# Kernel optimization log

Measured on AMD Instinct MI355X. Metric: run time of the kernel, lower is better.

Reference implementation:

```python
import jax, jax.numpy as jnp
import numpy as np

H, W = 720, 1280
NVIEWS, FEAT, HIDDEN = 30, 8, 64
GRIDS = ((16, 16, 8), (12, 12, 8), (8, 8, 4))  # (grid_X, grid_Y, grid_W) per scale
RGB2GRAY = np.array([0.299, 0.587, 0.114], dtype=np.float32)


def setup_inputs() -> dict:
    key = jax.random.key(0)
    ks = jax.random.split(key, 8)
    inp = {"rgb": jax.random.uniform(ks[0], (H, W, 3), jnp.float32)}
    for i, (gx, gy, gl) in enumerate(GRIDS):
        # grids: (N, C, L, Hg, Wg) per the docstring '(N, 12, L, H, W)'
        inp[f"grids{i}"] = jax.random.normal(ks[1 + i], (NVIEWS, FEAT, gl, gy, gx), jnp.float32) * 0.1
    din = len(GRIDS) * FEAT
    inp["w1"] = jax.random.normal(ks[4], (din, HIDDEN), jnp.float32) / np.sqrt(din)
    inp["w2"] = jax.random.normal(ks[5], (HIDDEN, HIDDEN), jnp.float32) / np.sqrt(HIDDEN)
    inp["w3"] = jax.random.normal(ks[6], (HIDDEN, 12), jnp.float32) / np.sqrt(HIDDEN)
    inp["cam_idx"] = 5
    return inp


def _slice_grid(g, rgb):
    """Trilinear bilateral-grid slicing (grid_sample 3D, align_corners=True).

    g: (C, L, Hg, Wg) grid for one view; rgb: (h, w, 3) in [0,1].
    Guidance z = gray luma; x/y are the normalized [0,1] image meshgrid.
    Returns (h, w, C).
    """
    C, L, Hg, Wg = g.shape
    h, w, _ = rgb.shape
    gray = jnp.clip(rgb @ jnp.asarray(RGB2GRAY, rgb.dtype), 0.0, 1.0)  # (h, w)
    # align_corners=True: normalized coord u in [0,1] -> u * (size - 1)
    x = jnp.broadcast_to(jnp.linspace(0.0, Wg - 1.0, w, dtype=rgb.dtype)[None, :], (h, w))
    y = jnp.broadcast_to(jnp.linspace(0.0, Hg - 1.0, h, dtype=rgb.dtype)[:, None], (h, w))
    z = gray * (L - 1.0)

    x0 = jnp.floor(x).astype(jnp.int32); x1 = jnp.minimum(x0 + 1, Wg - 1)
    y0 = jnp.floor(y).astype(jnp.int32); y1 = jnp.minimum(y0 + 1, Hg - 1)
    z0 = jnp.floor(z).astype(jnp.int32); z1 = jnp.minimum(z0 + 1, L - 1)
    wx, wy, wz = x - x0, y - y0, z - z0  # (h, w)

    def gat(zi, yi, xi):
        return g[:, zi, yi, xi]  # (C, h, w)

    c00 = gat(z0, y0, x0) * (1 - wx) + gat(z0, y0, x1) * wx
    c01 = gat(z0, y1, x0) * (1 - wx) + gat(z0, y1, x1) * wx
    c10 = gat(z1, y0, x0) * (1 - wx) + gat(z1, y0, x1) * wx
    c11 = gat(z1, y1, x0) * (1 - wx) + gat(z1, y1, x1) * wx
    c0 = c00 * (1 - wy) + c01 * wy
    c1 = c10 * (1 - wy) + c11 * wy
    out = c0 * (1 - wz) + c1 * wz  # (C, h, w)
    return jnp.transpose(out, (1, 2, 0))


def reference(rgb, grids0, grids1, grids2, w1, w2, w3, cam_idx):
    h, w, _ = rgb.shape
    feats = jnp.concatenate(
        [_slice_grid(g[cam_idx], rgb) for g in (grids0, grids1, grids2)], axis=-1
    )  # (h, w, 3*FEAT)
    hid = jnp.tanh(feats @ w1)
    hid = jnp.tanh(hid @ w2)
    out = hid @ w3  # (h, w, 12)
    return out.reshape(1, h, w, 3, 4)
```

## Files before the change

kernel.cpp:

```cpp
#include <hip/hip_runtime.h>
#include <hip/hip_bf16.h>

#define H_IMG 720
#define W_IMG 1280
#define NPIX (H_IMG * W_IMG)

typedef __attribute__((ext_vector_type(4))) float f32x4;
typedef __attribute__((ext_vector_type(8))) short short8;
typedef __attribute__((ext_vector_type(4))) short short4v;
typedef __attribute__((ext_vector_type(4))) uint u32x4;
typedef _Float16 h8 __attribute__((ext_vector_type(8)));

#define WPACK_BYTES (14 * 64 * 16)
#define GP0_OFF WPACK_BYTES
#define GP0_N (16 * 16 * 8 * 8)
#define GP1_OFF (GP0_OFF + GP0_N * 2)
#define GP1_N (12 * 12 * 8 * 8)
#define GP2_OFF (GP1_OFF + GP1_N * 2)
#define GP2_N (8 * 8 * 4 * 8)

#define XSTR 36

__device__ __forceinline__ uint pkh(float a, float b) {
  auto t = __builtin_amdgcn_cvt_pkrtz(a, b);
  return __builtin_bit_cast(uint, t);
}

__device__ __forceinline__ float tanh5(float x) {
  float e2 = __builtin_amdgcn_exp2f(x * 2.885390081777927f);
  return fmaf(-2.f, __builtin_amdgcn_rcpf(e2 + 1.f), 1.f);
}

__global__ __launch_bounds__(256) void prep_kernel(
    const float* __restrict__ g0, const float* __restrict__ g1, const float* __restrict__ g2,
    const float* __restrict__ w1, const float* __restrict__ w2, const float* __restrict__ w3,
    const int* __restrict__ cam, void* __restrict__ ws) {
  ushort* wpack = (ushort*)ws;
  ushort* gp0 = (ushort*)((char*)ws + GP0_OFF);
  ushort* gp1 = (ushort*)((char*)ws + GP1_OFF);
  ushort* gp2 = (ushort*)((char*)ws + GP2_OFF);
  const int ci = cam[0];
  const int tid = blockIdx.x * 256 + threadIdx.x;
  const int nth = gridDim.x * 256;

  for (int e = tid; e < GP0_N; e += nth) {
    int c = e & 7; int t = e >> 3; int z = t & 7; t >>= 3; int x = t & 15; int y = t >> 4;
    _Float16 hv = (_Float16)g0[ci * GP0_N + ((c * 8 + z) * 16 + y) * 16 + x];
    gp0[e] = __builtin_bit_cast(ushort, hv);
  }
  for (int e = tid; e < GP1_N; e += nth) {
    int c = e & 7; int t = e >> 3; int z = t & 7; t >>= 3; int x = t % 12; int y = t / 12;
    _Float16 hv = (_Float16)g1[ci * GP1_N + ((c * 8 + z) * 12 + y) * 12 + x];
    gp1[e] = __builtin_bit_cast(ushort, hv);
  }
  for (int e = tid; e < GP2_N; e += nth) {
    int c = e & 7; int t = e >> 3; int z = t & 3; t >>= 2; int x = t & 7; int y = t >> 3;
    _Float16 hv = (_Float16)g2[ci * GP2_N + ((c * 4 + z) * 8 + y) * 8 + x];
    gp2[e] = __builtin_bit_cast(ushort, hv);
  }

  for (int fl = tid; fl < 14 * 64; fl += nth) {
    int f = fl >> 6, lane = fl & 63;
    int g = lane >> 4, r = lane & 15;
    ushort* dh = wpack + fl * 8;
#pragma unroll
    for (int j = 0; j < 8; ++j) {
      float v = 0.f;
      if (f < 4) {
        int k = 8 * g + j, n = r + 16 * f;
        if (k < 24) v = w1[k * 64 + n];
      } else if (f < 12) {
        int q = f - 4, ks = q >> 2, mt = q & 3;
        v = w2[(8 * g + j + 32 * ks) * 64 + (r + 16 * mt)];
      } else {
        int ks = f - 12;
        if (r < 12) v = w3[(8 * g + j + 32 * ks) * 12 + r];
      }
      _Float16 hv = (_Float16)v;
      dh[j] = __builtin_bit_cast(ushort, hv);
    }
  }
}

template <int WG, int HG, int LG>
__device__ __forceinline__ h8 slice_h8(const h8* __restrict__ gp,
                                       int row, int col, float gray) {
  float x = (float)col * ((float)(WG - 1) / (float)(W_IMG - 1));
  float y = (float)row * ((float)(HG - 1) / (float)(H_IMG - 1));
  float z = gray * (float)(LG - 1);
  int x0 = (int)x, y0 = (int)y, z0 = (int)z;
  int x1 = min(x0 + 1, WG - 1), y1 = min(y0 + 1, HG - 1), z1 = min(z0 + 1, LG - 1);
  _Float16 wx = (_Float16)(x - (float)x0);
  _Float16 wy = (_Float16)(y - (float)y0);
  _Float16 wz = (_Float16)(z - (float)z0);
  h8 wx8 = {wx, wx, wx, wx, wx, wx, wx, wx};
  h8 wy8 = {wy, wy, wy, wy, wy, wy, wy, wy};
  h8 wz8 = {wz, wz, wz, wz, wz, wz, wz, wz};

  const h8* p00 = gp + (y0 * WG + x0) * LG;
  const h8* p01 = gp + (y0 * WG + x1) * LG;
  const h8* p10 = gp + (y1 * WG + x0) * LG;
  const h8* p11 = gp + (y1 * WG + x1) * LG;

  h8 a00 = p00[z0], a01 = p01[z0], a10 = p10[z0], a11 = p11[z0];
  h8 b00 = p00[z1], b01 = p01[z1], b10 = p10[z1], b11 = p11[z1];

  h8 xa = a00 + wx8 * (a01 - a00);
  h8 xb = a10 + wx8 * (a11 - a10);
  h8 ya = xa + wy8 * (xb - xa);
  h8 xc = b00 + wx8 * (b01 - b00);
  h8 xd = b10 + wx8 * (b11 - b10);
  h8 yb = xc + wy8 * (xd - xc);
  return ya + wz8 * (yb - ya);
}

__global__ __launch_bounds__(64, 4) void msnbat_kernel(
    const float* __restrict__ rgb, const void* __restrict__ ws, float* __restrict__ out) {
  __shared__ ushort W[64 * XSTR];
  uint* Wu = (uint*)W;

  const h8* wp = (const h8*)ws;
  const h8* gp0 = (const h8*)((const char*)ws + GP0_OFF);
  const h8* gp1 = (const h8*)((const char*)ws + GP1_OFF);
  const h8* gp2 = (const h8*)((const char*)ws + GP2_OFF);

  const int lane = threadIdx.x;
  const int g = lane >> 4, r = lane & 15;
  const int pixbase = blockIdx.x * 64;
  const int p = pixbase + lane;
  const int row = p / W_IMG;
  const int col = p - row * W_IMG;

  const float rr = rgb[p * 3 + 0], gg = rgb[p * 3 + 1], bb = rgb[p * 3 + 2];
  const float gray = fminf(fmaxf(rr * 0.299f + gg * 0.587f + bb * 0.114f, 0.f), 1.f);

  h8 f0 = slice_h8<16, 16, 8>(gp0, row, col, gray);
  h8 f1 = slice_h8<12, 12, 8>(gp1, row, col, gray);
  h8 f2 = slice_h8<8, 8, 4>(gp2, row, col, gray);

  {
    const int ub = lane * 18;
    u32x4 u0 = __builtin_bit_cast(u32x4, f0);
    u32x4 u1 = __builtin_bit_cast(u32x4, f1);
    u32x4 u2 = __builtin_bit_cast(u32x4, f2);
    *(uint2*)&Wu[ub + 0] = make_uint2(u0[0], u0[1]);
    *(uint2*)&Wu[ub + 2] = make_uint2(u0[2], u0[3]);
    *(uint2*)&Wu[ub + 4] = make_uint2(u1[0], u1[1]);
    *(uint2*)&Wu[ub + 6] = make_uint2(u1[2], u1[3]);
    *(uint2*)&Wu[ub + 8] = make_uint2(u2[0], u2[1]);
    *(uint2*)&Wu[ub + 10] = make_uint2(u2[2], u2[3]);
  }

  const h8 zero8 = (h8){0, 0, 0, 0, 0, 0, 0, 0};

  h8 B1[4];
#pragma unroll
  for (int nt = 0; nt < 4; ++nt) {
    short4v lo = *(short4v*)&W[(r + 16 * nt) * XSTR + 8 * g];
    short4v hi = *(short4v*)&W[(r + 16 * nt) * XSTR + 8 * g + 4];
    short8 s = __builtin_shufflevector(lo, hi, 0, 1, 2, 3, 4, 5, 6, 7);
    B1[nt] = (g < 3) ? __builtin_bit_cast(h8, s) : zero8;
  }

  h8 B2[2][4];
#pragma unroll
  for (int half = 0; half < 2; ++half) {
#pragma unroll
    for (int mtl = 0; mtl < 2; ++mtl) {
      const int mt = 2 * half + mtl;
      h8 A = wp[mt * 64 + lane];
      f32x4 a[4];
#pragma unroll
      for (int nt = 0; nt < 4; ++nt) a[nt] = (f32x4){0.f, 0.f, 0.f, 0.f};
#pragma unroll
      for (int nt = 0; nt < 4; ++nt)
        a[nt] = __builtin_amdgcn_mfma_f32_16x16x32_f16(A, B1[nt], a[nt], 0, 0, 0);
#pragma unroll
      for (int nt = 0; nt < 4; ++nt) {
        uint2 v = make_uint2(pkh(tanh5(a[nt][0]), tanh5(a[nt][1])),
                             pkh(tanh5(a[nt][2]), tanh5(a[nt][3])));
        *(uint2*)&Wu[(16 * nt + r) * 18 + 8 * mtl + 2 * g] = v;
      }
    }
#pragma unroll
    for (int nt = 0; nt < 4; ++nt) {
      short4v lo = *(short4v*)&W[(16 * nt + r) * XSTR + 8 * g];
      short4v hi = *(short4v*)&W[(16 * nt + r) * XSTR + 8 * g + 4];
      short8 s = __builtin_shufflevector(lo, hi, 0, 1, 2, 3, 4, 5, 6, 7);
      B2[half][nt] = __builtin_bit_cast(h8, s);
    }
  }

  h8 B3[2][4];
#pragma unroll
  for (int half = 0; half < 2; ++half) {
#pragma unroll
    for (int mtl = 0; mtl < 2; ++mtl) {
      const int mt = 2 * half + mtl;
      h8 A0 = wp[(4 + mt) * 64 + lane];
      h8 A1 = wp[(8 + mt) * 64 + lane];
      f32x4 a[4];
#pragma unroll
      for (int nt = 0; nt < 4; ++nt) a[nt] = (f32x4){0.f, 0.f, 0.f, 0.f};
#pragma unroll
      for (int nt = 0; nt < 4; ++nt)
        a[nt] = __builtin_amdgcn_mfma_f32_16x16x32_f16(A0, B2[0][nt], a[nt], 0, 0, 0);
#pragma unroll
      for (int nt = 0; nt < 4; ++nt)
        a[nt] = __builtin_amdgcn_mfma_f32_16x16x32_f16(A1, B2[1][nt], a[nt], 0, 0, 0);
#pragma unroll
      for (int nt = 0; nt < 4; ++nt) {
        uint2 v = make_uint2(pkh(tanh5(a[nt][0]), tanh5(a[nt][1])),
                             pkh(tanh5(a[nt][2]), tanh5(a[nt][3])));
        *(uint2*)&Wu[(16 * nt + r) * 18 + 8 * mtl + 2 * g] = v;
      }
    }
#pragma unroll
    for (int nt = 0; nt < 4; ++nt) {
      short4v lo = *(short4v*)&W[(16 * nt + r) * XSTR + 8 * g];
      short4v hi = *(short4v*)&W[(16 * nt + r) * XSTR + 8 * g + 4];
      short8 s = __builtin_shufflevector(lo, hi, 0, 1, 2, 3, 4, 5, 6, 7);
      B3[half][nt] = __builtin_bit_cast(h8, s);
    }
  }

  f32x4 acc3[4];
#pragma unroll
  for (int nt = 0; nt < 4; ++nt) acc3[nt] = (f32x4){0.f, 0.f, 0.f, 0.f};
  {
    h8 A0 = wp[12 * 64 + lane];
    h8 A1 = wp[13 * 64 + lane];
#pragma unroll
    for (int nt = 0; nt < 4; ++nt)
      acc3[nt] = __builtin_amdgcn_mfma_f32_16x16x32_f16(A0, B3[0][nt], acc3[nt], 0, 0, 0);
#pragma unroll
    for (int nt = 0; nt < 4; ++nt)
      acc3[nt] = __builtin_amdgcn_mfma_f32_16x16x32_f16(A1, B3[1][nt], acc3[nt], 0, 0, 0);
  }

  if (g < 3) {
#pragma unroll
    for (int nt = 0; nt < 4; ++nt) {
      int pix = pixbase + 16 * nt + r;
      *(f32x4*)(out + pix * 12 + 4 * g) = acc3[nt];
    }
  }
}

extern "C" void kernel_launch(void* const* d_in, const int* in_sizes, int n_in,
                              void* d_out, int out_size, void* d_ws, size_t ws_size,
                              hipStream_t stream) {
  const float* rgb = (const float*)d_in[0];
  const float* g0 = (const float*)d_in[1];
  const float* g1 = (const float*)d_in[2];
  const float* g2 = (const float*)d_in[3];
  const float* w1 = (const float*)d_in[4];
  const float* w2 = (const float*)d_in[5];
  const float* w3 = (const float*)d_in[6];
  const int* cam = (const int*)d_in[7];
  float* out = (float*)d_out;

  hipLaunchKernelGGL(prep_kernel, dim3(64), dim3(256), 0, stream,
                     g0, g1, g2, w1, w2, w3, cam, d_ws);
  hipLaunchKernelGGL(msnbat_kernel, dim3(NPIX / 64), dim3(64), 0, stream,
                     rgb, d_ws, out);
}
```

Measured before the change: 53.78 us.

## Widen LDS hidden buffer to full 64 rows and fold tanh scale into weights

Folds the 2/ln2 tanh pre-scale into the packed w1/w2 weights during prep, which removes one multiply per activation. The hidden-layer staging buffer is widened so each layer computes all four M-tiles before writing tanh results, replacing the earlier two-halves interleave. This lengthens MFMA chains and drops intermediate LDS round trips. In exchange, accumulator register pressure rises (16 f32x4 live per layer) and the LDS footprint roughly doubles, which may lower occupancy.

```diff
diff --git a/kernel.cpp b/kernel.cpp
--- a/kernel.cpp
+++ b/kernel.cpp
@@ -19,16 +19,23 @@
 #define GP2_OFF (GP1_OFF + GP1_N * 2)
 #define GP2_N (8 * 8 * 4 * 8)
 
-#define XSTR 36
+#define HSTR 68
+
+#define KSCALE 2.885390081777927f
 
 __device__ __forceinline__ uint pkh(float a, float b) {
   auto t = __builtin_amdgcn_cvt_pkrtz(a, b);
   return __builtin_bit_cast(uint, t);
 }
 
-__device__ __forceinline__ float tanh5(float x) {
-  float e2 = __builtin_amdgcn_exp2f(x * 2.885390081777927f);
-  return fmaf(-2.f, __builtin_amdgcn_rcpf(e2 + 1.f), 1.f);
+__device__ __forceinline__ float tanhu(float u) {
+  float e2 = __builtin_amdgcn_exp2f(u);
+  float r = __builtin_amdgcn_rcpf(e2 + 1.f);
+  return fmaf(-2.f, r, 1.f);
+}
+
+__device__ __forceinline__ uint2 tanh4(f32x4 u) {
+  return make_uint2(pkh(tanhu(u[0]), tanhu(u[1])), pkh(tanhu(u[2]), tanhu(u[3])));
 }
 
 __global__ __launch_bounds__(256) void prep_kernel(
@@ -68,10 +75,10 @@
       float v = 0.f;
       if (f < 4) {
         int k = 8 * g + j, n = r + 16 * f;
-        if (k < 24) v = w1[k * 64 + n];
+        if (k < 24) v = w1[k * 64 + n] * KSCALE;
       } else if (f < 12) {
         int q = f - 4, ks = q >> 2, mt = q & 3;
-        v = w2[(8 * g + j + 32 * ks) * 64 + (r + 16 * mt)];
+        v = w2[(8 * g + j + 32 * ks) * 64 + (r + 16 * mt)] * KSCALE;
       } else {
         int ks = f - 12;
         if (r < 12) v = w3[(8 * g + j + 32 * ks) * 12 + r];
@@ -116,7 +123,7 @@
 
 __global__ __launch_bounds__(64, 4) void msnbat_kernel(
     const float* __restrict__ rgb, const void* __restrict__ ws, float* __restrict__ out) {
-  __shared__ ushort W[64 * XSTR];
+  __shared__ ushort W[64 * HSTR];
   uint* Wu = (uint*)W;
 
   const h8* wp = (const h8*)ws;
@@ -139,7 +146,7 @@
   h8 f2 = slice_h8<8, 8, 4>(gp2, row, col, gray);
 
   {
-    const int ub = lane * 18;
+    const int ub = lane * (HSTR / 2);
     u32x4 u0 = __builtin_bit_cast(u32x4, f0);
     u32x4 u1 = __builtin_bit_cast(u32x4, f1);
     u32x4 u2 = __builtin_bit_cast(u32x4, f2);
@@ -156,86 +163,79 @@
   h8 B1[4];
 #pragma unroll
   for (int nt = 0; nt < 4; ++nt) {
-    short4v lo = *(short4v*)&W[(r + 16 * nt) * XSTR + 8 * g];
-    short4v hi = *(short4v*)&W[(r + 16 * nt) * XSTR + 8 * g + 4];
+    short4v lo = *(short4v*)&W[(r + 16 * nt) * HSTR + 8 * g];
+    short4v hi = *(short4v*)&W[(r + 16 * nt) * HSTR + 8 * g + 4];
     short8 s = __builtin_shufflevector(lo, hi, 0, 1, 2, 3, 4, 5, 6, 7);
     B1[nt] = (g < 3) ? __builtin_bit_cast(h8, s) : zero8;
   }
 
+  {
+    f32x4 a1[4][4];
+#pragma unroll
+    for (int mt = 0; mt < 4; ++mt)
+#pragma unroll
+      for (int nt = 0; nt < 4; ++nt) a1[mt][nt] = (f32x4){0.f, 0.f, 0.f, 0.f};
+#pragma unroll
+    for (int mt = 0; mt < 4; ++mt) {
+      h8 A = wp[mt * 64 + lane];
+#pragma unroll
+      for (int nt = 0; nt < 4; ++nt)
+        a1[mt][nt] = __builtin_amdgcn_mfma_f32_16x16x32_f16(A, B1[nt], a1[mt][nt], 0, 0, 0);
+    }
+#pragma unroll
+    for (int mt = 0; mt < 4; ++mt)
+#pragma unroll
+      for (int nt = 0; nt < 4; ++nt)
+        *(uint2*)&Wu[(16 * nt + r) * (HSTR / 2) + 8 * mt + 2 * g] = tanh4(a1[mt][nt]);
+  }
+
   h8 B2[2][4];
 #pragma unroll
-  for (int half = 0; half < 2; ++half) {
-#pragma unroll
-    for (int mtl = 0; mtl < 2; ++mtl) {
-      const int mt = 2 * half + mtl;
-      h8 A = wp[mt * 64 + lane];
-      f32x4 a[4];
-#pragma unroll
-      for (int nt = 0; nt < 4; ++nt) a[nt] = (f32x4){0.f, 0.f, 0.f, 0.f};
+  for (int ks = 0; ks < 2; ++ks)
+#pragma unroll
+    for (int nt = 0; nt < 4; ++nt) {
+      short4v lo = *(short4v*)&W[(16 * nt + r) * HSTR + 32 * ks + 8 * g];
+      short4v hi = *(short4v*)&W[(16 * nt + r) * HSTR + 32 * ks + 8 * g + 4];
+      short8 s = __builtin_shufflevector(lo, hi, 0, 1, 2, 3, 4, 5, 6, 7);
+      B2[ks][nt] = __builtin_bit_cast(h8, s);
+    }
+
+  {
+    f32x4 a2[4][4];
+#pragma unroll
+    for (int mt = 0; mt < 4; ++mt)
+#pragma unroll
+      for (int nt = 0; nt < 4; ++nt) a2[mt][nt] = (f32x4){0.f, 0.f, 0.f, 0.f};
+#pragma unroll
+    for (int ks = 0; ks < 2; ++ks)
+#pragma unroll
+      for (int mt = 0; mt < 4; ++mt) {
+        h8 A = wp[(4 + ks * 4 + mt) * 64 + lane];
+#pragma unroll
+        for (int nt = 0; nt < 4; ++nt)
+          a2[mt][nt] = __builtin_amdgcn_mfma_f32_16x16x32_f16(A, B2[ks][nt], a2[mt][nt], 0, 0, 0);
+      }
+#pragma unroll
+    for (int mt = 0; mt < 4; ++mt)
 #pragma unroll
       for (int nt = 0; nt < 4; ++nt)
-        a[nt] = __builtin_amdgcn_mfma_f32_16x16x32_f16(A, B1[nt], a[nt], 0, 0, 0);
-#pragma unroll
-      for (int nt = 0; nt < 4; ++nt) {
-        uint2 v = make_uint2(pkh(tanh5(a[nt][0]), tanh5(a[nt][1])),
-                             pkh(tanh5(a[nt][2]), tanh5(a[nt][3])));
-        *(uint2*)&Wu[(16 * nt + r) * 18 + 8 * mtl + 2 * g] = v;
-      }
-    }
+        *(uint2*)&Wu[(16 * nt + r) * (HSTR / 2) + 8 * mt + 2 * g] = tanh4(a2[mt][nt]);
+  }
+
+  f32x4 acc3[4];
+#pragma unroll
+  for (int nt = 0; nt < 4; ++nt) acc3[nt] = (f32x4){0.f, 0.f, 0.f, 0.f};
+#pragma unroll
+  for (int ks = 0; ks < 2; ++ks) {
+    h8 A = wp[(12 + ks) * 64 + lane];
 #pragma unroll
     for (int nt = 0; nt < 4; ++nt) {
-      short4v lo = *(short4v*)&W[(16 * nt + r) * XSTR + 8 * g];
-      short4v hi = *(short4v*)&W[(16 * nt + r) * XSTR + 8 * g + 4];
+      short4v lo = *(short4v*)&W[(16 * nt + r) * HSTR + 32 * ks + 8 * g];
+      short4v hi = *(short4v*)&W[(16 * nt + r) * HSTR + 32 * ks + 8 * g + 4];
       short8 s = __builtin_shufflevector(lo, hi, 0, 1, 2, 3, 4, 5, 6, 7);
-      B2[half][nt] = __builtin_bit_cast(h8, s);
-    }
-  }
-
-  h8 B3[2][4];
-#pragma unroll
-  for (int half = 0; half < 2; ++half) {
-#pragma unroll
-    for (int mtl = 0; mtl < 2; ++mtl) {
-      const int mt = 2 * half + mtl;
-      h8 A0 = wp[(4 + mt) * 64 + lane];
-      h8 A1 = wp[(8 + mt) * 64 + lane];
-      f32x4 a[4];
-#pragma unroll
-      for (int nt = 0; nt < 4; ++nt) a[nt] = (f32x4){0.f, 0.f, 0.f, 0.f};
-#pragma unroll
-      for (int nt = 0; nt < 4; ++nt)
-        a[nt] = __builtin_amdgcn_mfma_f32_16x16x32_f16(A0, B2[0][nt], a[nt], 0, 0, 0);
-#pragma unroll
-      for (int nt = 0; nt < 4; ++nt)
-        a[nt] = __builtin_amdgcn_mfma_f32_16x16x32_f16(A1, B2[1][nt], a[nt], 0, 0, 0);
-#pragma unroll
-      for (int nt = 0; nt < 4; ++nt) {
-        uint2 v = make_uint2(pkh(tanh5(a[nt][0]), tanh5(a[nt][1])),
-                             pkh(tanh5(a[nt][2]), tanh5(a[nt][3])));
-        *(uint2*)&Wu[(16 * nt + r) * 18 + 8 * mtl + 2 * g] = v;
-      }
-    }
-#pragma unroll
-    for (int nt = 0; nt < 4; ++nt) {
-      short4v lo = *(short4v*)&W[(16 * nt + r) * XSTR + 8 * g];
-      short4v hi = *(short4v*)&W[(16 * nt + r) * XSTR + 8 * g + 4];
-      short8 s = __builtin_shufflevector(lo, hi, 0, 1, 2, 3, 4, 5, 6, 7);
-      B3[half][nt] = __builtin_bit_cast(h8, s);
-    }
-  }
-
-  f32x4 acc3[4];
-#pragma unroll
-  for (int nt = 0; nt < 4; ++nt) acc3[nt] = (f32x4){0.f, 0.f, 0.f, 0.f};
-  {
-    h8 A0 = wp[12 * 64 + lane];
-    h8 A1 = wp[13 * 64 + lane];
-#pragma unroll
-    for (int nt = 0; nt < 4; ++nt)
-      acc3[nt] = __builtin_amdgcn_mfma_f32_16x16x32_f16(A0, B3[0][nt], acc3[nt], 0, 0, 0);
-#pragma unroll
-    for (int nt = 0; nt < 4; ++nt)
-      acc3[nt] = __builtin_amdgcn_mfma_f32_16x16x32_f16(A1, B3[1][nt], acc3[nt], 0, 0, 0);
+      h8 B = __builtin_bit_cast(h8, s);
+      acc3[nt] = __builtin_amdgcn_mfma_f32_16x16x32_f16(A, B, acc3[nt], 0, 0, 0);
+    }
   }
 
   if (g < 3) {
```

Measured after the change: 51.63 us. -4.0%, faster.
